# Kernel tuning notes

Hardware: AMD Instinct MI355X
Metric: run time of the kernel (lower is better)

## Reference

```python
import jax, jax.numpy as jnp
import numpy as np
from jax import lax

B, N, C = 16, 2304, 768
H_HEADS, D = 12, 64  # num_heads, head_dim
SCALE = 9.0 ** (-0.5)  # equivalent_head_dim ** -0.5


def setup_inputs() -> dict:
    key = jax.random.key(0)
    ks = jax.random.split(key, 8)
    return {
        "x": jax.random.normal(ks[0], (B, N, C), dtype=jnp.float32),
        "qkv_w": jax.random.normal(ks[1], (3 * C + 3 * D, C), dtype=jnp.float32) * 0.02,
        "qkv_b": jax.random.normal(ks[2], (3 * C + 3 * D,), dtype=jnp.float32) * 0.02,
        "w1": jax.random.normal(ks[3], (1, H_HEADS, D, D), dtype=jnp.float32) * 0.02,
        "w2": jax.random.normal(ks[4], (1, H_HEADS, D, D), dtype=jnp.float32) * 0.02,
        "w3": jax.random.normal(ks[5], (D, 1, 3, 3), dtype=jnp.float32) * 0.02,
        "proj_w": jax.random.normal(ks[6], (C, C + D), dtype=jnp.float32) * 0.02,
        "proj_b": jax.random.normal(ks[7], (C,), dtype=jnp.float32) * 0.02,
        "h": 48,
        "w": 48,
    }


def _inner_swiglu(k, v, w1, w2, lr=1.0):
    # k, v: [B, H, N, d]; w1, w2: [1, H, d, d]
    z1 = jnp.einsum('bhnd,hde->bhne', k, w1[0])
    z2 = jnp.einsum('bhnd,hde->bhne', k, w2[0])
    sig = jax.nn.sigmoid(z2)
    a = z2 * sig
    e = -v / float(v.shape[2]) * SCALE
    g1 = jnp.einsum('bhnd,bhne->bhde', k, e * a)
    g2 = jnp.einsum('bhnd,bhne->bhde', k, e * z1 * (sig * (1.0 + z2 * (1.0 - sig))))
    g1 = g1 / (jnp.linalg.norm(g1, axis=-2, keepdims=True) + 1.0)
    g2 = g2 / (jnp.linalg.norm(g2, axis=-2, keepdims=True) + 1.0)
    return w1 - lr * g1, w2 - lr * g2  # [B, H, d, d]


def _inner_3x3dwc(k, v, w3, hh, ww, lr=1.0):
    # k, v: [B, d, h, w]; w3: [d, 1, 3, 3]
    b, c = k.shape[0], k.shape[1]
    e = -v / float(hh * ww) * SCALE
    kp = jnp.pad(k, ((0, 0), (0, 0), (1, 1), (1, 1)))
    dots = []
    for ys in (0, 1, 2):  # 1 + dy
        for xs in (0, 1, 2):  # 1 + dx
            dots.append(jnp.sum(kp[:, :, ys:ys + hh, xs:xs + ww] * e, axis=(-2, -1)))
    g = jnp.stack(dots, axis=-1).reshape(b * c, 1, 3, 3)
    g = g / (jnp.sqrt(jnp.sum(g * g, axis=(-2, -1), keepdims=True)) + 1.0)
    return jnp.tile(w3, (b, 1, 1, 1)) - lr * g  # [B*d, 1, 3, 3]


def reference(x, qkv_w, qkv_b, w1, w2, w3, proj_w, proj_b, h, w):
    b, n, c = x.shape
    nh = w1.shape[1]
    d = c // nh
    qkv = x @ qkv_w.T + qkv_b  # [B, N, 3C + 3d]
    q1, k1, v1, q2, k2, v2 = jnp.split(
        qkv, [c, 2 * c, 3 * c, 3 * c + d, 3 * c + 2 * d], axis=-1)
    heads = lambda t: t.reshape(b, n, nh, d).transpose(0, 2, 1, 3)
    q1, k1, v1 = heads(q1), heads(k1), heads(v1)

    w1u, w2u = _inner_swiglu(k1, v1, w1, w2)
    x1 = jnp.einsum('bhnd,bhde->bhne', q1, w1u) * jax.nn.silu(
        jnp.einsum('bhnd,bhde->bhne', q1, w2u))
    x1 = x1.transpose(0, 2, 1, 3).reshape(b, n, c)

    spatial = lambda t: t.reshape(b, h, w, d).transpose(0, 3, 1, 2)  # [B, d, h, w]
    q2s, k2s, v2s = spatial(q2), spatial(k2), spatial(v2)
    w3u = _inner_3x3dwc(k2s, v2s, w3, h, w)
    x2 = lax.conv_general_dilated(
        q2s.reshape(1, b * d, h, w), w3u,
        window_strides=(1, 1), padding=((1, 1), (1, 1)),
        feature_group_count=b * d,
        dimension_numbers=('NCHW', 'OIHW', 'NCHW'))
    x2 = x2.reshape(b, d, n).transpose(0, 2, 1)  # [B, N, d]

    out = jnp.concatenate([x1, x2], axis=-1) @ proj_w.T + proj_b
    return out
```

## Files before the change

kernel.cpp:

```cpp
#include <hip/hip_runtime.h>
#include <hip/hip_bf16.h>
#include <math.h>

#define B_   16
#define N_   2304
#define C_   768
#define H_   12
#define D_   64
#define M_   (B_*N_)
#define NQKV 2496
#define NPAD 2560
#define CCP  896
#define EVS  (-1.0f/6912.0f)

typedef __bf16 bf16x8 __attribute__((ext_vector_type(8)));
typedef __bf16 bf16x4 __attribute__((ext_vector_type(4)));
typedef float  f32x4  __attribute__((ext_vector_type(4)));

static __device__ __forceinline__ void gload_lds16(const void* g, void* l) {
  __builtin_amdgcn_global_load_lds((const __attribute__((address_space(1))) void*)g,
                                   (__attribute__((address_space(3))) void*)l, 16, 0, 0);
}

static __device__ __forceinline__ bf16x8 ld8(const __bf16* p) {
  bf16x4 lo = *(const bf16x4*)p;
  bf16x4 hi = *(const bf16x4*)(p + 4);
  return __builtin_shufflevector(lo, hi, 0,1,2,3,4,5,6,7);
}

__global__ __launch_bounds__(256) void cvt_x(const float* __restrict__ in,
                                             __bf16* __restrict__ out, int n8) {
  int i = blockIdx.x * 256 + threadIdx.x;
  if (i >= n8) return;
  const float4* p = (const float4*)(in + (size_t)i * 8);
  float4 a = p[0], b = p[1];
  bf16x8 o = {(__bf16)a.x,(__bf16)a.y,(__bf16)a.z,(__bf16)a.w,
              (__bf16)b.x,(__bf16)b.y,(__bf16)b.z,(__bf16)b.w};
  *(bf16x8*)(out + (size_t)i * 8) = o;
}

__global__ __launch_bounds__(256) void cvt_wqkv(const float* __restrict__ w,
    const float* __restrict__ bias, __bf16* __restrict__ wout, float* __restrict__ bout) {
  int i = blockIdx.x * 256 + threadIdx.x;
  if (i < NPAD * 96) {
    int n = i / 96, c8 = i - n * 96;
    bf16x8 o;
    if (n < NQKV) {
      const float4* p = (const float4*)(w + (size_t)n * 768 + c8 * 8);
      float4 a = p[0], b = p[1];
      o = (bf16x8){(__bf16)a.x,(__bf16)a.y,(__bf16)a.z,(__bf16)a.w,
                   (__bf16)b.x,(__bf16)b.y,(__bf16)b.z,(__bf16)b.w};
    } else {
      o = (bf16x8){(__bf16)0.f,(__bf16)0.f,(__bf16)0.f,(__bf16)0.f,
                   (__bf16)0.f,(__bf16)0.f,(__bf16)0.f,(__bf16)0.f};
    }
    *(bf16x8*)(wout + (size_t)n * 768 + c8 * 8) = o;
  }
  if (i < NPAD) bout[i] = (i < NQKV) ? bias[i] : 0.0f;
}

__global__ __launch_bounds__(256) void cvt_pw(const float* __restrict__ in,
                                              __bf16* __restrict__ out) {
  int i = blockIdx.x * 256 + threadIdx.x;
  if (i >= 86016) return;
  int n = i / 112, c8 = i - n * 112;
  int k = c8 * 8;
  bf16x8 o;
  if (k < 832) {
    const float4* p = (const float4*)(in + (size_t)n * 832 + k);
    float4 a = p[0], b = p[1];
    o = (bf16x8){(__bf16)a.x,(__bf16)a.y,(__bf16)a.z,(__bf16)a.w,
                 (__bf16)b.x,(__bf16)b.y,(__bf16)b.z,(__bf16)b.w};
  } else {
    o = (bf16x8){(__bf16)0.f,(__bf16)0.f,(__bf16)0.f,(__bf16)0.f,
                 (__bf16)0.f,(__bf16)0.f,(__bf16)0.f,(__bf16)0.f};
  }
  *(bf16x8*)(out + (size_t)n * CCP + k) = o;
}

__global__ __launch_bounds__(256) void zeropad(__bf16* __restrict__ concat) {
  int i = blockIdx.x * 256 + threadIdx.x;
  if (i >= M_ * 8) return;
  int row = i >> 3, ch = i & 7;
  bf16x8 z = {(__bf16)0.f,(__bf16)0.f,(__bf16)0.f,(__bf16)0.f,
              (__bf16)0.f,(__bf16)0.f,(__bf16)0.f,(__bf16)0.f};
  *(bf16x8*)(concat + (size_t)row * CCP + 832 + ch * 8) = z;
}

template<int OUTF32>
__global__ __launch_bounds__(512, 2) void gemm8(
    const __bf16* __restrict__ A, const __bf16* __restrict__ Bt,
    const float* __restrict__ bias, void* __restrict__ Cout,
    const int K, const int ldc, const int nbn, const int KT)
{
  __shared__ __align__(16) __bf16 sA[2][2][128 * 64];
  __shared__ __align__(16) __bf16 sB[2][2][128 * 64];
  const int tid  = threadIdx.x;
  const int lane = tid & 63;
  const int wid  = tid >> 6;
  const int wm = wid >> 2;
  const int wn = wid & 3;
  const int l15 = lane & 15, lq = lane >> 4;

  const int nwg = gridDim.x;
  const int swz = ((int)blockIdx.x & 7) * (nwg >> 3) + ((int)blockIdx.x >> 3);
  const int bm = swz / nbn;
  const int bn = swz - bm * nbn;

  const int strow = tid >> 3;
  const int stoff = strow * 64 + (tid & 7) * 8;
  const __bf16* gA = A  + (size_t)((size_t)bm * 256 + strow) * K + ((tid & 7) ^ (strow & 7)) * 8;
  const __bf16* gB = Bt + (size_t)((size_t)bn * 256 + strow) * K + ((tid & 7) ^ (strow & 7)) * 8;

  f32x4 acc[2][4][2][2];
  #pragma unroll
  for (int a = 0; a < 2; ++a)
    #pragma unroll
    for (int m = 0; m < 4; ++m)
      #pragma unroll
      for (int b = 0; b < 2; ++b)
        #pragma unroll
        for (int n = 0; n < 2; ++n) acc[a][m][b][n] = (f32x4){0.f,0.f,0.f,0.f};

  bf16x8 af0[4][2], af1[4][2], bf0[2][2], bf1[2][2];

#define STAGE_A(q, h, T) do {                                                   \
    const size_t ko_ = (size_t)(T) * 64;                                        \
    gload_lds16(gA + (size_t)((h)*128 +  0) * K + ko_, &sA[q][h][stoff]);       \
    gload_lds16(gA + (size_t)((h)*128 + 64) * K + ko_, &sA[q][h][4096 + stoff]);\
  } while (0)
#define STAGE_B(q, h, T) do {                                                   \
    const size_t ko_ = (size_t)(T) * 64;                                        \
    gload_lds16(gB + (size_t)((h)*128 +  0) * K + ko_, &sB[q][h][stoff]);       \
    gload_lds16(gB + (size_t)((h)*128 + 64) * K + ko_, &sB[q][h][4096 + stoff]);\
  } while (0)
#define LOADA(DST, h, q) do {                                                   \
    _Pragma("unroll") for (int mf_ = 0; mf_ < 4; ++mf_) {                       \
      const int r_ = wm * 64 + mf_ * 16 + l15;                                  \
      _Pragma("unroll") for (int kk_ = 0; kk_ < 2; ++kk_)                       \
        DST[mf_][kk_] = *(const bf16x8*)&sA[q][h][r_ * 64 + (((kk_*4+lq) ^ (r_&7)) * 8)]; \
    } } while (0)
#define LOADB(DST, h, q) do {                                                   \
    _Pragma("unroll") for (int nf_ = 0; nf_ < 2; ++nf_) {                       \
      const int c_ = wn * 32 + nf_ * 16 + l15;                                  \
      _Pragma("unroll") for (int kk_ = 0; kk_ < 2; ++kk_)                       \
        DST[nf_][kk_] = *(const bf16x8*)&sB[q][h][c_ * 64 + (((kk_*4+lq) ^ (c_&7)) * 8)]; \
    } } while (0)
#define MMA(a_, b_, AF, BF) do {                                                \
    __builtin_amdgcn_s_setprio(1);                                              \
    _Pragma("unroll") for (int kk_ = 0; kk_ < 2; ++kk_)                         \
    _Pragma("unroll") for (int mf_ = 0; mf_ < 4; ++mf_)                         \
    _Pragma("unroll") for (int nf_ = 0; nf_ < 2; ++nf_)                         \
      acc[a_][mf_][b_][nf_] = __builtin_amdgcn_mfma_f32_16x16x32_bf16(          \
          AF[mf_][kk_], BF[nf_][kk_], acc[a_][mf_][b_][nf_], 0, 0, 0);          \
    __builtin_amdgcn_s_setprio(0);                                              \
  } while (0)
#define BAR  __builtin_amdgcn_s_barrier()
#define LGKM do { asm volatile("s_waitcnt lgkmcnt(0)" ::: "memory");            \
                  __builtin_amdgcn_sched_barrier(0); } while (0)
#define VMW4 asm volatile("s_waitcnt vmcnt(4)" ::: "memory")
#define VMW0 asm volatile("s_waitcnt vmcnt(0)" ::: "memory")

  STAGE_A(0, 0, 0); STAGE_A(0, 1, 0); STAGE_B(0, 0, 0); STAGE_B(0, 1, 0);
  STAGE_B(1, 0, 1);
  STAGE_A(1, 1, 1);
  VMW4;
  BAR;

  for (int t = 0; t < KT; t += 2) {
    LOADA(af0, 0, 0); LOADB(bf0, 0, 0);
    STAGE_A(1, 0, t + 1); STAGE_B(1, 1, t + 1);
    BAR; LGKM; MMA(0, 0, af0, bf0); BAR;
    LOADA(af1, 1, 0);
    BAR; LGKM; MMA(1, 0, af1, bf0); BAR;
    LOADB(bf1, 1, 0);
    if (t + 2 < KT) STAGE_B(0, 0, t + 2);
    BAR; LGKM; MMA(1, 1, af1, bf1); BAR;
    if (t + 2 < KT) STAGE_A(0, 1, t + 2);
    BAR; MMA(0, 1, af0, bf1);
    if (t + 2 < KT) { VMW4; } else { VMW0; }
    BAR;
    LOADA(af0, 0, 1); LOADB(bf0, 0, 1);
    if (t + 2 < KT) { STAGE_A(0, 0, t + 2); STAGE_B(0, 1, t + 2); }
    BAR; LGKM; MMA(0, 0, af0, bf0); BAR;
    LOADA(af1, 1, 1);
    BAR; LGKM; MMA(1, 0, af1, bf0); BAR;
    LOADB(bf1, 1, 1);
    if (t + 3 < KT) STAGE_B(1, 0, t + 3);
    BAR; LGKM; MMA(1, 1, af1, bf1); BAR;
    if (t + 3 < KT) STAGE_A(1, 1, t + 3);
    BAR; MMA(0, 1, af0, bf1);
    if (t + 3 < KT) { VMW4; } else { VMW0; }
    BAR;
  }
#undef STAGE_A
#undef STAGE_B
#undef LOADA
#undef LOADB
#undef MMA

  #pragma unroll
  for (int b = 0; b < 2; ++b)
    #pragma unroll
    for (int nf = 0; nf < 2; ++nf) {
      const int col = bn * 256 + b * 128 + wn * 32 + nf * 16 + l15;
      const float bs = bias[col];
      #pragma unroll
      for (int a = 0; a < 2; ++a)
        #pragma unroll
        for (int mf = 0; mf < 4; ++mf) {
          const int row0 = bm * 256 + a * 128 + wm * 64 + mf * 16 + lq * 4;
          #pragma unroll
          for (int r = 0; r < 4; ++r) {
            float v = acc[a][mf][b][nf][r] + bs;
            if (OUTF32) ((float*)Cout)[(size_t)(row0 + r) * ldc + col] = v;
            else        ((__bf16*)Cout)[(size_t)(row0 + r) * ldc + col] = (__bf16)v;
          }
        }
    }
}

__global__ __launch_bounds__(256, 2) void inner_swiglu(
    const __bf16* __restrict__ qkv, const float* __restrict__ w1,
    const float* __restrict__ w2, __bf16* __restrict__ concat)
{
  const int bh = blockIdx.x;
  const int b = bh / H_, h = bh - b * H_;
  const int tid = threadIdx.x, wid = tid >> 6, lane = tid & 63;
  const int wr = wid >> 1, wc = wid & 1, l15 = lane & 15, lq = lane >> 4;

  __shared__ __bf16 w1T[64 * 72], w2T[64 * 72];
  __shared__ union U {
    struct { __bf16 kN[64 * 72], kT[64 * 72], t1T[64 * 72], t2T[64 * 72]; } c;
    struct { float g1[64 * 65], g2[64 * 65]; float nrm1[64], nrm2[64]; } g;
  } u;

  const float* w1p = w1 + h * 4096;
  const float* w2p = w2 + h * 4096;
  for (int idx = tid; idx < 4096; idx += 256) {
    int d = idx >> 6, e = idx & 63;
    w1T[e * 72 + d] = (__bf16)w1p[idx];
    w2T[e * 72 + d] = (__bf16)w2p[idx];
  }

  f32x4 g1a[2][2], g2a[2][2];
  #pragma unroll
  for (int i = 0; i < 2; ++i)
    #pragma unroll
    for (int j = 0; j < 2; ++j) { g1a[i][j] = (f32x4){0.f,0.f,0.f,0.f}; g2a[i][j] = (f32x4){0.f,0.f,0.f,0.f}; }

  const size_t rowb = (size_t)b * N_;
  const int koff = C_ + h * D_;
  const int voff = 2 * C_ + h * D_;
  __syncthreads();

  const int sn = tid >> 2, sdb = tid & 3;

  for (int ci = 0; ci < 36; ++ci) {
    const int n0 = ci * 64;
    {
      const __bf16* src = qkv + (rowb + n0 + sn) * (size_t)NPAD + koff + sdb * 16;
      bf16x8 va = *(const bf16x8*)src;
      bf16x8 vb = *(const bf16x8*)(src + 8);
      __bf16* kn = &u.c.kN[sn * 72 + sdb * 16];
      *(bf16x4*)(kn + 0)  = __builtin_shufflevector(va, va, 0,1,2,3);
      *(bf16x4*)(kn + 4)  = __builtin_shufflevector(va, va, 4,5,6,7);
      *(bf16x4*)(kn + 8)  = __builtin_shufflevector(vb, vb, 0,1,2,3);
      *(bf16x4*)(kn + 12) = __builtin_shufflevector(vb, vb, 4,5,6,7);
      #pragma unroll
      for (int j = 0; j < 8; ++j) u.c.kT[(sdb * 16 + j) * 72 + sn] = va[j];
      #pragma unroll
      for (int j = 0; j < 8; ++j) u.c.kT[(sdb * 16 + 8 + j) * 72 + sn] = vb[j];
    }
    __syncthreads();

    f32x4 z1[2][2], z2[2][2];
    #pragma unroll
    for (int i = 0; i < 2; ++i)
      #pragma unroll
      for (int j = 0; j < 2; ++j) { z1[i][j] = (f32x4){0.f,0.f,0.f,0.f}; z2[i][j] = (f32x4){0.f,0.f,0.f,0.f}; }
    #pragma unroll
    for (int kk = 0; kk < 2; ++kk) {
      bf16x8 af[2], b1[2], b2[2];
      #pragma unroll
      for (int mi = 0; mi < 2; ++mi)
        af[mi] = ld8(&u.c.kN[(wr * 32 + mi * 16 + l15) * 72 + kk * 32 + lq * 8]);
      #pragma unroll
      for (int ni = 0; ni < 2; ++ni) {
        int e = wc * 32 + ni * 16 + l15;
        b1[ni] = ld8(&w1T[e * 72 + kk * 32 + lq * 8]);
        b2[ni] = ld8(&w2T[e * 72 + kk * 32 + lq * 8]);
      }
      #pragma unroll
      for (int mi = 0; mi < 2; ++mi)
        #pragma unroll
        for (int ni = 0; ni < 2; ++ni) {
          z1[mi][ni] = __builtin_amdgcn_mfma_f32_16x16x32_bf16(af[mi], b1[ni], z1[mi][ni], 0, 0, 0);
          z2[mi][ni] = __builtin_amdgcn_mfma_f32_16x16x32_bf16(af[mi], b2[ni], z2[mi][ni], 0, 0, 0);
        }
    }

    #pragma unroll
    for (int mi = 0; mi < 2; ++mi)
      #pragma unroll
      for (int ni = 0; ni < 2; ++ni) {
        int nl = wr * 32 + mi * 16 + lq * 4;
        int e  = wc * 32 + ni * 16 + l15;
        const __bf16* vp = qkv + (rowb + n0 + nl) * (size_t)NPAD + voff + e;
        #pragma unroll
        for (int r = 0; r < 4; ++r) {
          float vv  = (float)vp[(size_t)r * NPAD];
          float ev  = vv * EVS;
          float z1v = z1[mi][ni][r], z2v = z2[mi][ni][r];
          float sg  = 1.0f / (1.0f + __expf(-z2v));
          float t1  = ev * (z2v * sg);
          float t2  = ev * z1v * (sg * (1.0f + z2v * (1.0f - sg)));
          u.c.t1T[e * 72 + nl + r] = (__bf16)t1;
          u.c.t2T[e * 72 + nl + r] = (__bf16)t2;
        }
      }
    __syncthreads();

    #pragma unroll
    for (int kk = 0; kk < 2; ++kk) {
      bf16x8 af[2], b1[2], b2[2];
      #pragma unroll
      for (int mi = 0; mi < 2; ++mi)
        af[mi] = ld8(&u.c.kT[(wr * 32 + mi * 16 + l15) * 72 + kk * 32 + lq * 8]);
      #pragma unroll
      for (int ni = 0; ni < 2; ++ni) {
        int e = wc * 32 + ni * 16 + l15;
        b1[ni] = ld8(&u.c.t1T[e * 72 + kk * 32 + lq * 8]);
        b2[ni] = ld8(&u.c.t2T[e * 72 + kk * 32 + lq * 8]);
      }
      #pragma unroll
      for (int mi = 0; mi < 2; ++mi)
        #pragma unroll
        for (int ni = 0; ni < 2; ++ni) {
          g1a[mi][ni] = __builtin_amdgcn_mfma_f32_16x16x32_bf16(af[mi], b1[ni], g1a[mi][ni], 0, 0, 0);
          g2a[mi][ni] = __builtin_amdgcn_mfma_f32_16x16x32_bf16(af[mi], b2[ni], g2a[mi][ni], 0, 0, 0);
        }
    }
    __syncthreads();
  }

  #pragma unroll
  for (int mi = 0; mi < 2; ++mi)
    #pragma unroll
    for (int ni = 0; ni < 2; ++ni)
      #pragma unroll
      for (int r = 0; r < 4; ++r) {
        int d = wr * 32 + mi * 16 + lq * 4 + r;
        int e = wc * 32 + ni * 16 + l15;
        u.g.g1[d * 65 + e] = g1a[mi][ni][r];
        u.g.g2[d * 65 + e] = g2a[mi][ni][r];
      }
  __syncthreads();
  if (tid < 128) {
    const float* gs = (tid < 64) ? u.g.g1 : u.g.g2;
    int e = tid & 63;
    float s = 0.f;
    for (int d = 0; d < 64; ++d) { float gv = gs[d * 65 + e]; s += gv * gv; }
    float rn = 1.0f / (sqrtf(s) + 1.0f);
    if (tid < 64) u.g.nrm1[e] = rn; else u.g.nrm2[e] = rn;
  }
  __syncthreads();
  for (int idx = tid; idx < 4096; idx += 256) {
    int d = idx >> 6, e = idx & 63;
    float wu1 = w1p[idx] - u.g.g1[d * 65 + e] * u.g.nrm1[e];
    float wu2 = w2p[idx] - u.g.g2[d * 65 + e] * u.g.nrm2[e];
    w1T[e * 72 + d] = (__bf16)wu1;
    w2T[e * 72 + d] = (__bf16)wu2;
  }
  __syncthreads();

  const int qoff = h * D_;
  for (int ci = 0; ci < 36; ++ci) {
    const int n0 = ci * 64;
    {
      const __bf16* src = qkv + (rowb + n0 + sn) * (size_t)NPAD + qoff + sdb * 16;
      bf16x8 va = *(const bf16x8*)src;
      bf16x8 vb = *(const bf16x8*)(src + 8);
      __bf16* kn = &u.c.kN[sn * 72 + sdb * 16];
      *(bf16x4*)(kn + 0)  = __builtin_shufflevector(va, va, 0,1,2,3);
      *(bf16x4*)(kn + 4)  = __builtin_shufflevector(va, va, 4,5,6,7);
      *(bf16x4*)(kn + 8)  = __builtin_shufflevector(vb, vb, 0,1,2,3);
      *(bf16x4*)(kn + 12) = __builtin_shufflevector(vb, vb, 4,5,6,7);
    }
    __syncthreads();
    f32x4 y1[2][2], y2[2][2];
    #pragma unroll
    for (int i = 0; i < 2; ++i)
      #pragma unroll
      for (int j = 0; j < 2; ++j) { y1[i][j] = (f32x4){0.f,0.f,0.f,0.f}; y2[i][j] = (f32x4){0.f,0.f,0.f,0.f}; }
    #pragma unroll
    for (int kk = 0; kk < 2; ++kk) {
      bf16x8 af[2], b1[2], b2[2];
      #pragma unroll
      for (int mi = 0; mi < 2; ++mi)
        af[mi] = ld8(&u.c.kN[(wr * 32 + mi * 16 + l15) * 72 + kk * 32 + lq * 8]);
      #pragma unroll
      for (int ni = 0; ni < 2; ++ni) {
        int e = wc * 32 + ni * 16 + l15;
        b1[ni] = ld8(&w1T[e * 72 + kk * 32 + lq * 8]);
        b2[ni] = ld8(&w2T[e * 72 + kk * 32 + lq * 8]);
      }
      #pragma unroll
      for (int mi = 0; mi < 2; ++mi)
        #pragma unroll
        for (int ni = 0; ni < 2; ++ni) {
          y1[mi][ni] = __builtin_amdgcn_mfma_f32_16x16x32_bf16(af[mi], b1[ni], y1[mi][ni], 0, 0, 0);
          y2[mi][ni] = __builtin_amdgcn_mfma_f32_16x16x32_bf16(af[mi], b2[ni], y2[mi][ni], 0, 0, 0);
        }
    }
    #pragma unroll
    for (int mi = 0; mi < 2; ++mi)
      #pragma unroll
      for (int ni = 0; ni < 2; ++ni) {
        int nl = wr * 32 + mi * 16 + lq * 4;
        int e  = wc * 32 + ni * 16 + l15;
        #pragma unroll
        for (int r = 0; r < 4; ++r) {
          float a1 = y1[mi][ni][r], a2 = y2[mi][ni][r];
          float sg = 1.0f / (1.0f + __expf(-a2));
          concat[(rowb + n0 + nl + r) * (size_t)CCP + h * D_ + e] = (__bf16)(a1 * (a2 * sg));
        }
      }
    __syncthreads();
  }
}

__global__ __launch_bounds__(256) void dwc_grad(const __bf16* __restrict__ qkv,
    const float* __restrict__ w3, float* __restrict__ w3u) {
  int bd = blockIdx.x, b = bd >> 6, dd = bd & 63;
  int tid = threadIdx.x;
  __shared__ float kpad[50 * 50];
  __shared__ float red[9][4];
  for (int i = tid; i < 2500; i += 256) kpad[i] = 0.f;
  __syncthreads();
  const size_t base = (size_t)b * N_ * NPAD;
  for (int p = tid; p < 2304; p += 256) {
    int y = p / 48, x = p - y * 48;
    kpad[(y + 1) * 50 + x + 1] = (float)qkv[base + (size_t)p * NPAD + 2368 + dd];
  }
  __syncthreads();
  float acc[9];
  #pragma unroll
  for (int j = 0; j < 9; ++j) acc[j] = 0.f;
  for (int p = tid; p < 2304; p += 256) {
    int y = p / 48, x = p - y * 48;
    float e = (float)qkv[base + (size_t)p * NPAD + 2432 + dd] * EVS;
    #pragma unroll
    for (int j = 0; j < 9; ++j) {
      int ys = j / 3, xs = j - ys * 3;
      acc[j] += kpad[(y + ys) * 50 + (x + xs)] * e;
    }
  }
  #pragma unroll
  for (int j = 0; j < 9; ++j)
    for (int off = 32; off; off >>= 1) acc[j] += __shfl_down(acc[j], off);
  if ((tid & 63) == 0) {
    #pragma unroll
    for (int j = 0; j < 9; ++j) red[j][tid >> 6] = acc[j];
  }
  __syncthreads();
  if (tid == 0) {
    float g[9]; float ss = 0.f;
    #pragma unroll
    for (int j = 0; j < 9; ++j) {
      g[j] = red[j][0] + red[j][1] + red[j][2] + red[j][3];
      ss += g[j] * g[j];
    }
    float rn = 1.0f / (sqrtf(ss) + 1.0f);
    #pragma unroll
    for (int j = 0; j < 9; ++j) w3u[bd * 9 + j] = w3[dd * 9 + j] - g[j] * rn;
  }
}

__global__ __launch_bounds__(256) void dwc_apply(const __bf16* __restrict__ qkv,
    const float* __restrict__ w3u, __bf16* __restrict__ concat) {
  int bd = blockIdx.x, b = bd >> 6, dd = bd & 63;
  int tid = threadIdx.x;
  __shared__ float qpad[50 * 50];
  for (int i = tid; i < 2500; i += 256) qpad[i] = 0.f;
  __syncthreads();
  const size_t base = (size_t)b * N_ * NPAD;
  for (int p = tid; p < 2304; p += 256) {
    int y = p / 48, x = p - y * 48;
    qpad[(y + 1) * 50 + x + 1] = (float)qkv[base + (size_t)p * NPAD + 2304 + dd];
  }
  __syncthreads();
  float wv[9];
  #pragma unroll
  for (int j = 0; j < 9; ++j) wv[j] = w3u[bd * 9 + j];
  for (int p = tid; p < 2304; p += 256) {
    int y = p / 48, x = p - y * 48;
    float s = 0.f;
    #pragma unroll
    for (int j = 0; j < 9; ++j) {
      int ys = j / 3, xs = j - ys * 3;
      s += qpad[(y + ys) * 50 + (x + xs)] * wv[j];
    }
    concat[((size_t)b * N_ + p) * CCP + 768 + dd] = (__bf16)s;
  }
}

extern "C" void kernel_launch(void* const* d_in, const int* in_sizes, int n_in,
                              void* d_out, int out_size, void* d_ws, size_t ws_size,
                              hipStream_t stream) {
  const float* x      = (const float*)d_in[0];
  const float* qkv_w  = (const float*)d_in[1];
  const float* qkv_b  = (const float*)d_in[2];
  const float* w1     = (const float*)d_in[3];
  const float* w2     = (const float*)d_in[4];
  const float* w3     = (const float*)d_in[5];
  const float* proj_w = (const float*)d_in[6];
  const float* proj_b = (const float*)d_in[7];

  char* ws = (char*)d_ws;
  __bf16* xb     = (__bf16*)ws;
  __bf16* wqkvb  = (__bf16*)(ws + 56623104);
  float*  qkvbp  = (float*) (ws + 60555264);
  __bf16* concat = (__bf16*)ws;
  __bf16* qkvb16 = (__bf16*)(ws + 66060288);
  __bf16* pwb    = (__bf16*)(ws + 254803968);
  float*  w3u    = (float*) (ws + 256180224);

  cvt_x   <<<13824, 256, 0, stream>>>(x, xb, 3538944);
  cvt_wqkv<<<  960, 256, 0, stream>>>(qkv_w, qkv_b, wqkvb, qkvbp);
  cvt_pw  <<<  336, 256, 0, stream>>>(proj_w, pwb);

  gemm8<0><<<1440, 512, 0, stream>>>(xb, wqkvb, qkvbp, (void*)qkvb16,
                                     768, NPAD, 10, 12);

  zeropad<<<1152, 256, 0, stream>>>(concat);
  inner_swiglu<<<192, 256, 0, stream>>>(qkvb16, w1, w2, concat);
  dwc_grad <<<1024, 256, 0, stream>>>(qkvb16, w3, w3u);
  dwc_apply<<<1024, 256, 0, stream>>>(qkvb16, w3u, concat);

  gemm8<1><<<432, 512, 0, stream>>>(concat, pwb, proj_b, d_out,
                                    CCP, 768, 3, 14);
}
```

Baseline: 485.3 us.

## Rework GEMM wait scheduling, split swiglu over two groups, retile depthwise conv kernels

Three separate changes. The GEMM main loop drops its explicit lgkmcnt waits and puts sched_barrier fences after barriers and vmcnt waits. inner_swiglu moves to 512 threads, with two wave groups handling alternate 64-token chunks; V is staged through LDS, and the two groups' gradient partials are summed in shared memory. The depthwise conv gradient and apply kernels change from one block per (batch, channel) with strided scalar loads to blocks over 4-row spatial strips that read all 64 channels with vectorized loads, plus a small reduction kernel for the per-strip partial gradients. Removing the lgkmcnt waits leaves it to the compiler to wait for the LDS fragment loads before the MFMAs, which carries a correctness risk.

```diff
diff --git a/kernel.cpp b/kernel.cpp
--- a/kernel.cpp
+++ b/kernel.cpp
@@ -155,11 +155,12 @@
           AF[mf_][kk_], BF[nf_][kk_], acc[a_][mf_][b_][nf_], 0, 0, 0);          \
     __builtin_amdgcn_s_setprio(0);                                              \
   } while (0)
-#define BAR  __builtin_amdgcn_s_barrier()
-#define LGKM do { asm volatile("s_waitcnt lgkmcnt(0)" ::: "memory");            \
+#define BAR  do { __builtin_amdgcn_s_barrier();                                 \
                   __builtin_amdgcn_sched_barrier(0); } while (0)
-#define VMW4 asm volatile("s_waitcnt vmcnt(4)" ::: "memory")
-#define VMW0 asm volatile("s_waitcnt vmcnt(0)" ::: "memory")
+#define VMW4 do { asm volatile("s_waitcnt vmcnt(4)" ::: "memory");              \
+                  __builtin_amdgcn_sched_barrier(0); } while (0)
+#define VMW0 do { asm volatile("s_waitcnt vmcnt(0)" ::: "memory");              \
+                  __builtin_amdgcn_sched_barrier(0); } while (0)
 
   STAGE_A(0, 0, 0); STAGE_A(0, 1, 0); STAGE_B(0, 0, 0); STAGE_B(0, 1, 0);
   STAGE_B(1, 0, 1);
@@ -170,24 +171,24 @@
   for (int t = 0; t < KT; t += 2) {
     LOADA(af0, 0, 0); LOADB(bf0, 0, 0);
     STAGE_A(1, 0, t + 1); STAGE_B(1, 1, t + 1);
-    BAR; LGKM; MMA(0, 0, af0, bf0); BAR;
+    BAR; MMA(0, 0, af0, bf0); BAR;
     LOADA(af1, 1, 0);
-    BAR; LGKM; MMA(1, 0, af1, bf0); BAR;
+    BAR; MMA(1, 0, af1, bf0); BAR;
     LOADB(bf1, 1, 0);
     if (t + 2 < KT) STAGE_B(0, 0, t + 2);
-    BAR; LGKM; MMA(1, 1, af1, bf1); BAR;
+    BAR; MMA(1, 1, af1, bf1); BAR;
     if (t + 2 < KT) STAGE_A(0, 1, t + 2);
     BAR; MMA(0, 1, af0, bf1);
     if (t + 2 < KT) { VMW4; } else { VMW0; }
     BAR;
     LOADA(af0, 0, 1); LOADB(bf0, 0, 1);
     if (t + 2 < KT) { STAGE_A(0, 0, t + 2); STAGE_B(0, 1, t + 2); }
-    BAR; LGKM; MMA(0, 0, af0, bf0); BAR;
+    BAR; MMA(0, 0, af0, bf0); BAR;
     LOADA(af1, 1, 1);
-    BAR; LGKM; MMA(1, 0, af1, bf0); BAR;
+    BAR; MMA(1, 0, af1, bf0); BAR;
     LOADB(bf1, 1, 1);
     if (t + 3 < KT) STAGE_B(1, 0, t + 3);
-    BAR; LGKM; MMA(1, 1, af1, bf1); BAR;
+    BAR; MMA(1, 1, af1, bf1); BAR;
     if (t + 3 < KT) STAGE_A(1, 1, t + 3);
     BAR; MMA(0, 1, af0, bf1);
     if (t + 3 < KT) { VMW4; } else { VMW0; }
@@ -220,24 +221,27 @@
     }
 }
 
-__global__ __launch_bounds__(256, 2) void inner_swiglu(
+__global__ __launch_bounds__(512, 1) void inner_swiglu(
     const __bf16* __restrict__ qkv, const float* __restrict__ w1,
     const float* __restrict__ w2, __bf16* __restrict__ concat)
 {
   const int bh = blockIdx.x;
   const int b = bh / H_, h = bh - b * H_;
   const int tid = threadIdx.x, wid = tid >> 6, lane = tid & 63;
-  const int wr = wid >> 1, wc = wid & 1, l15 = lane & 15, lq = lane >> 4;
+  const int grp = wid >> 2;
+  const int wid2 = wid & 3;
+  const int wr = wid2 >> 1, wc = wid2 & 1, l15 = lane & 15, lq = lane >> 4;
 
   __shared__ __bf16 w1T[64 * 72], w2T[64 * 72];
   __shared__ union U {
-    struct { __bf16 kN[64 * 72], kT[64 * 72], t1T[64 * 72], t2T[64 * 72]; } c;
+    struct { __bf16 kN[2][64 * 72], kT[2][64 * 72], vN[2][64 * 72],
+                    t1T[2][64 * 72], t2T[2][64 * 72]; } c;
     struct { float g1[64 * 65], g2[64 * 65]; float nrm1[64], nrm2[64]; } g;
   } u;
 
   const float* w1p = w1 + h * 4096;
   const float* w2p = w2 + h * 4096;
-  for (int idx = tid; idx < 4096; idx += 256) {
+  for (int idx = tid; idx < 4096; idx += 512) {
     int d = idx >> 6, e = idx & 63;
     w1T[e * 72 + d] = (__bf16)w1p[idx];
     w2T[e * 72 + d] = (__bf16)w2p[idx];
@@ -252,25 +256,31 @@
   const size_t rowb = (size_t)b * N_;
   const int koff = C_ + h * D_;
   const int voff = 2 * C_ + h * D_;
-  __syncthreads();
-
-  const int sn = tid >> 2, sdb = tid & 3;
-
-  for (int ci = 0; ci < 36; ++ci) {
-    const int n0 = ci * 64;
+  const int st = tid & 255, sn = st >> 2, sdb = st & 3;
+
+  for (int it = 0; it < 18; ++it) {
+    const int n0 = (it * 2 + grp) * 64;
     {
       const __bf16* src = qkv + (rowb + n0 + sn) * (size_t)NPAD + koff + sdb * 16;
       bf16x8 va = *(const bf16x8*)src;
       bf16x8 vb = *(const bf16x8*)(src + 8);
-      __bf16* kn = &u.c.kN[sn * 72 + sdb * 16];
+      __bf16* kn = &u.c.kN[grp][sn * 72 + sdb * 16];
       *(bf16x4*)(kn + 0)  = __builtin_shufflevector(va, va, 0,1,2,3);
       *(bf16x4*)(kn + 4)  = __builtin_shufflevector(va, va, 4,5,6,7);
       *(bf16x4*)(kn + 8)  = __builtin_shufflevector(vb, vb, 0,1,2,3);
       *(bf16x4*)(kn + 12) = __builtin_shufflevector(vb, vb, 4,5,6,7);
       #pragma unroll
-      for (int j = 0; j < 8; ++j) u.c.kT[(sdb * 16 + j) * 72 + sn] = va[j];
-      #pragma unroll
-      for (int j = 0; j < 8; ++j) u.c.kT[(sdb * 16 + 8 + j) * 72 + sn] = vb[j];
+      for (int j = 0; j < 8; ++j) u.c.kT[grp][(sdb * 16 + j) * 72 + sn] = va[j];
+      #pragma unroll
+      for (int j = 0; j < 8; ++j) u.c.kT[grp][(sdb * 16 + 8 + j) * 72 + sn] = vb[j];
+      const __bf16* vsrc = qkv + (rowb + n0 + sn) * (size_t)NPAD + voff + sdb * 16;
+      bf16x8 wa = *(const bf16x8*)vsrc;
+      bf16x8 wb = *(const bf16x8*)(vsrc + 8);
+      __bf16* vn = &u.c.vN[grp][sn * 72 + sdb * 16];
+      *(bf16x4*)(vn + 0)  = __builtin_shufflevector(wa, wa, 0,1,2,3);
+      *(bf16x4*)(vn + 4)  = __builtin_shufflevector(wa, wa, 4,5,6,7);
+      *(bf16x4*)(vn + 8)  = __builtin_shufflevector(wb, wb, 0,1,2,3);
+      *(bf16x4*)(vn + 12) = __builtin_shufflevector(wb, wb, 4,5,6,7);
     }
     __syncthreads();
 
@@ -284,7 +294,7 @@
       bf16x8 af[2], b1[2], b2[2];
       #pragma unroll
       for (int mi = 0; mi < 2; ++mi)
-        af[mi] = ld8(&u.c.kN[(wr * 32 + mi * 16 + l15) * 72 + kk * 32 + lq * 8]);
+        af[mi] = ld8(&u.c.kN[grp][(wr * 32 + mi * 16 + l15) * 72 + kk * 32 + lq * 8]);
       #pragma unroll
       for (int ni = 0; ni < 2; ++ni) {
         int e = wc * 32 + ni * 16 + l15;
@@ -306,17 +316,16 @@
       for (int ni = 0; ni < 2; ++ni) {
         int nl = wr * 32 + mi * 16 + lq * 4;
         int e  = wc * 32 + ni * 16 + l15;
-        const __bf16* vp = qkv + (rowb + n0 + nl) * (size_t)NPAD + voff + e;
         #pragma unroll
         for (int r = 0; r < 4; ++r) {
-          float vv  = (float)vp[(size_t)r * NPAD];
+          float vv  = (float)u.c.vN[grp][(nl + r) * 72 + e];
           float ev  = vv * EVS;
           float z1v = z1[mi][ni][r], z2v = z2[mi][ni][r];
           float sg  = 1.0f / (1.0f + __expf(-z2v));
           float t1  = ev * (z2v * sg);
           float t2  = ev * z1v * (sg * (1.0f + z2v * (1.0f - sg)));
-          u.c.t1T[e * 72 + nl + r] = (__bf16)t1;
-          u.c.t2T[e * 72 + nl + r] = (__bf16)t2;
+          u.c.t1T[grp][e * 72 + nl + r] = (__bf16)t1;
+          u.c.t2T[grp][e * 72 + nl + r] = (__bf16)t2;
         }
       }
     __syncthreads();
@@ -326,12 +335,12 @@
       bf16x8 af[2], b1[2], b2[2];
       #pragma unroll
       for (int mi = 0; mi < 2; ++mi)
-        af[mi] = ld8(&u.c.kT[(wr * 32 + mi * 16 + l15) * 72 + kk * 32 + lq * 8]);
+        af[mi] = ld8(&u.c.kT[grp][(wr * 32 + mi * 16 + l15) * 72 + kk * 32 + lq * 8]);
       #pragma unroll
       for (int ni = 0; ni < 2; ++ni) {
         int e = wc * 32 + ni * 16 + l15;
-        b1[ni] = ld8(&u.c.t1T[e * 72 + kk * 32 + lq * 8]);
-        b2[ni] = ld8(&u.c.t2T[e * 72 + kk * 32 + lq * 8]);
+        b1[ni] = ld8(&u.c.t1T[grp][e * 72 + kk * 32 + lq * 8]);
+        b2[ni] = ld8(&u.c.t2T[grp][e * 72 + kk * 32 + lq * 8]);
       }
       #pragma unroll
       for (int mi = 0; mi < 2; ++mi)
@@ -344,17 +353,33 @@
     __syncthreads();
   }
 
-  #pragma unroll
-  for (int mi = 0; mi < 2; ++mi)
-    #pragma unroll
-    for (int ni = 0; ni < 2; ++ni)
-      #pragma unroll
-      for (int r = 0; r < 4; ++r) {
-        int d = wr * 32 + mi * 16 + lq * 4 + r;
-        int e = wc * 32 + ni * 16 + l15;
-        u.g.g1[d * 65 + e] = g1a[mi][ni][r];
-        u.g.g2[d * 65 + e] = g2a[mi][ni][r];
-      }
+  if (grp == 0) {
+    #pragma unroll
+    for (int mi = 0; mi < 2; ++mi)
+      #pragma unroll
+      for (int ni = 0; ni < 2; ++ni)
+        #pragma unroll
+        for (int r = 0; r < 4; ++r) {
+          int d = wr * 32 + mi * 16 + lq * 4 + r;
+          int e = wc * 32 + ni * 16 + l15;
+          u.g.g1[d * 65 + e] = g1a[mi][ni][r];
+          u.g.g2[d * 65 + e] = g2a[mi][ni][r];
+        }
+  }
+  __syncthreads();
+  if (grp == 1) {
+    #pragma unroll
+    for (int mi = 0; mi < 2; ++mi)
+      #pragma unroll
+      for (int ni = 0; ni < 2; ++ni)
+        #pragma unroll
+        for (int r = 0; r < 4; ++r) {
+          int d = wr * 32 + mi * 16 + lq * 4 + r;
+          int e = wc * 32 + ni * 16 + l15;
+          u.g.g1[d * 65 + e] += g1a[mi][ni][r];
+          u.g.g2[d * 65 + e] += g2a[mi][ni][r];
+        }
+  }
   __syncthreads();
   if (tid < 128) {
     const float* gs = (tid < 64) ? u.g.g1 : u.g.g2;
@@ -365,7 +390,7 @@
     if (tid < 64) u.g.nrm1[e] = rn; else u.g.nrm2[e] = rn;
   }
   __syncthreads();
-  for (int idx = tid; idx < 4096; idx += 256) {
+  for (int idx = tid; idx < 4096; idx += 512) {
     int d = idx >> 6, e = idx & 63;
     float wu1 = w1p[idx] - u.g.g1[d * 65 + e] * u.g.nrm1[e];
     float wu2 = w2p[idx] - u.g.g2[d * 65 + e] * u.g.nrm2[e];
@@ -375,13 +400,13 @@
   __syncthreads();
 
   const int qoff = h * D_;
-  for (int ci = 0; ci < 36; ++ci) {
-    const int n0 = ci * 64;
+  for (int it = 0; it < 18; ++it) {
+    const int n0 = (it * 2 + grp) * 64;
     {
       const __bf16* src = qkv + (rowb + n0 + sn) * (size_t)NPAD + qoff + sdb * 16;
       bf16x8 va = *(const bf16x8*)src;
       bf16x8 vb = *(const bf16x8*)(src + 8);
-      __bf16* kn = &u.c.kN[sn * 72 + sdb * 16];
+      __bf16* kn = &u.c.kN[grp][sn * 72 + sdb * 16];
       *(bf16x4*)(kn + 0)  = __builtin_shufflevector(va, va, 0,1,2,3);
       *(bf16x4*)(kn + 4)  = __builtin_shufflevector(va, va, 4,5,6,7);
       *(bf16x4*)(kn + 8)  = __builtin_shufflevector(vb, vb, 0,1,2,3);
@@ -398,7 +423,7 @@
       bf16x8 af[2], b1[2], b2[2];
       #pragma unroll
       for (int mi = 0; mi < 2; ++mi)
-        af[mi] = ld8(&u.c.kN[(wr * 32 + mi * 16 + l15) * 72 + kk * 32 + lq * 8]);
+        af[mi] = ld8(&u.c.kN[grp][(wr * 32 + mi * 16 + l15) * 72 + kk * 32 + lq * 8]);
       #pragma unroll
       for (int ni = 0; ni < 2; ++ni) {
         int e = wc * 32 + ni * 16 + l15;
@@ -430,77 +455,102 @@
   }
 }
 
-__global__ __launch_bounds__(256) void dwc_grad(const __bf16* __restrict__ qkv,
-    const float* __restrict__ w3, float* __restrict__ w3u) {
-  int bd = blockIdx.x, b = bd >> 6, dd = bd & 63;
-  int tid = threadIdx.x;
-  __shared__ float kpad[50 * 50];
-  __shared__ float red[9][4];
-  for (int i = tid; i < 2500; i += 256) kpad[i] = 0.f;
+__global__ __launch_bounds__(256) void dwc_grad2(const __bf16* __restrict__ qkv,
+                                                 float* __restrict__ w3p) {
+  const int blk = blockIdx.x;
+  const int b = blk / 12, sp = blk - b * 12;
+  const int tid = threadIdx.x, dd = tid & 63, rl = tid >> 6;
+  __shared__ __bf16 kS[6 * 50 * 64];
+  __shared__ float red[4][9][64];
+  for (int i = tid; i < 9600; i += 256) ((unsigned*)kS)[i] = 0u;
   __syncthreads();
   const size_t base = (size_t)b * N_ * NPAD;
-  for (int p = tid; p < 2304; p += 256) {
-    int y = p / 48, x = p - y * 48;
-    kpad[(y + 1) * 50 + x + 1] = (float)qkv[base + (size_t)p * NPAD + 2368 + dd];
+  for (int i = tid; i < 6 * 48 * 8; i += 256) {
+    int y6 = i / 384; int rem = i - y6 * 384; int x = rem >> 3; int c8 = rem & 7;
+    int y = 4 * sp - 1 + y6;
+    if (y >= 0 && y < 48) {
+      int p = y * 48 + x;
+      bf16x8 v = *(const bf16x8*)&qkv[base + (size_t)p * NPAD + 2368 + c8 * 8];
+      *(bf16x8*)&kS[((y6 * 50) + x + 1) * 64 + c8 * 8] = v;
+    }
   }
   __syncthreads();
   float acc[9];
   #pragma unroll
   for (int j = 0; j < 9; ++j) acc[j] = 0.f;
-  for (int p = tid; p < 2304; p += 256) {
-    int y = p / 48, x = p - y * 48;
+  const int y = 4 * sp + rl;
+  for (int x = 0; x < 48; ++x) {
+    int p = y * 48 + x;
     float e = (float)qkv[base + (size_t)p * NPAD + 2432 + dd] * EVS;
     #pragma unroll
     for (int j = 0; j < 9; ++j) {
       int ys = j / 3, xs = j - ys * 3;
-      acc[j] += kpad[(y + ys) * 50 + (x + xs)] * e;
-    }
-  }
-  #pragma unroll
-  for (int j = 0; j < 9; ++j)
-    for (int off = 32; off; off >>= 1) acc[j] += __shfl_down(acc[j], off);
-  if ((tid & 63) == 0) {
-    #pragma unroll
-    for (int j = 0; j < 9; ++j) red[j][tid >> 6] = acc[j];
-  }
-  __syncthreads();
-  if (tid == 0) {
-    float g[9]; float ss = 0.f;
+      acc[j] += (float)kS[((rl + ys) * 50 + x + xs) * 64 + dd] * e;
+    }
+  }
+  #pragma unroll
+  for (int j = 0; j < 9; ++j) red[rl][j][dd] = acc[j];
+  __syncthreads();
+  if (rl == 0) {
     #pragma unroll
     for (int j = 0; j < 9; ++j) {
-      g[j] = red[j][0] + red[j][1] + red[j][2] + red[j][3];
-      ss += g[j] * g[j];
-    }
-    float rn = 1.0f / (sqrtf(ss) + 1.0f);
-    #pragma unroll
-    for (int j = 0; j < 9; ++j) w3u[bd * 9 + j] = w3[dd * 9 + j] - g[j] * rn;
-  }
-}
-
-__global__ __launch_bounds__(256) void dwc_apply(const __bf16* __restrict__ qkv,
+      float s = red[0][j][dd] + red[1][j][dd] + red[2][j][dd] + red[3][j][dd];
+      w3p[((size_t)(b * 12 + sp) * 64 + dd) * 9 + j] = s;
+    }
+  }
+}
+
+__global__ __launch_bounds__(256) void dwc_upd(const float* __restrict__ w3p,
+    const float* __restrict__ w3, float* __restrict__ w3u) {
+  int i = blockIdx.x * 256 + threadIdx.x;
+  if (i >= 1024) return;
+  int b = i >> 6, dd = i & 63;
+  float g[9];
+  #pragma unroll
+  for (int j = 0; j < 9; ++j) g[j] = 0.f;
+  for (int sp = 0; sp < 12; ++sp)
+    #pragma unroll
+    for (int j = 0; j < 9; ++j)
+      g[j] += w3p[((size_t)(b * 12 + sp) * 64 + dd) * 9 + j];
+  float ss = 0.f;
+  #pragma unroll
+  for (int j = 0; j < 9; ++j) ss += g[j] * g[j];
+  float rn = 1.0f / (sqrtf(ss) + 1.0f);
+  #pragma unroll
+  for (int j = 0; j < 9; ++j) w3u[i * 9 + j] = w3[dd * 9 + j] - g[j] * rn;
+}
+
+__global__ __launch_bounds__(256) void dwc_apply2(const __bf16* __restrict__ qkv,
     const float* __restrict__ w3u, __bf16* __restrict__ concat) {
-  int bd = blockIdx.x, b = bd >> 6, dd = bd & 63;
-  int tid = threadIdx.x;
-  __shared__ float qpad[50 * 50];
-  for (int i = tid; i < 2500; i += 256) qpad[i] = 0.f;
+  const int blk = blockIdx.x;
+  const int b = blk / 12, sp = blk - b * 12;
+  const int tid = threadIdx.x, dd = tid & 63, rl = tid >> 6;
+  __shared__ __bf16 qS[6 * 50 * 64];
+  for (int i = tid; i < 9600; i += 256) ((unsigned*)qS)[i] = 0u;
   __syncthreads();
   const size_t base = (size_t)b * N_ * NPAD;
-  for (int p = tid; p < 2304; p += 256) {
-    int y = p / 48, x = p - y * 48;
-    qpad[(y + 1) * 50 + x + 1] = (float)qkv[base + (size_t)p * NPAD + 2304 + dd];
+  for (int i = tid; i < 6 * 48 * 8; i += 256) {
+    int y6 = i / 384; int rem = i - y6 * 384; int x = rem >> 3; int c8 = rem & 7;
+    int y = 4 * sp - 1 + y6;
+    if (y >= 0 && y < 48) {
+      int p = y * 48 + x;
+      bf16x8 v = *(const bf16x8*)&qkv[base + (size_t)p * NPAD + 2304 + c8 * 8];
+      *(bf16x8*)&qS[((y6 * 50) + x + 1) * 64 + c8 * 8] = v;
+    }
   }
   __syncthreads();
   float wv[9];
   #pragma unroll
-  for (int j = 0; j < 9; ++j) wv[j] = w3u[bd * 9 + j];
-  for (int p = tid; p < 2304; p += 256) {
-    int y = p / 48, x = p - y * 48;
+  for (int j = 0; j < 9; ++j) wv[j] = w3u[(size_t)(b * 64 + dd) * 9 + j];
+  const int y = 4 * sp + rl;
+  for (int x = 0; x < 48; ++x) {
     float s = 0.f;
     #pragma unroll
     for (int j = 0; j < 9; ++j) {
       int ys = j / 3, xs = j - ys * 3;
-      s += qpad[(y + ys) * 50 + (x + xs)] * wv[j];
-    }
+      s += (float)qS[((rl + ys) * 50 + x + xs) * 64 + dd] * wv[j];
+    }
+    int p = y * 48 + x;
     concat[((size_t)b * N_ + p) * CCP + 768 + dd] = (__bf16)s;
   }
 }
@@ -525,6 +575,7 @@
   __bf16* qkvb16 = (__bf16*)(ws + 66060288);
   __bf16* pwb    = (__bf16*)(ws + 254803968);
   float*  w3u    = (float*) (ws + 256180224);
+  float*  w3p    = (float*) (ws + 256217088);
 
   cvt_x   <<<13824, 256, 0, stream>>>(x, xb, 3538944);
   cvt_wqkv<<<  960, 256, 0, stream>>>(qkv_w, qkv_b, wqkvb, qkvbp);
@@ -534,9 +585,10 @@
                                      768, NPAD, 10, 12);
 
   zeropad<<<1152, 256, 0, stream>>>(concat);
-  inner_swiglu<<<192, 256, 0, stream>>>(qkvb16, w1, w2, concat);
-  dwc_grad <<<1024, 256, 0, stream>>>(qkvb16, w3, w3u);
-  dwc_apply<<<1024, 256, 0, stream>>>(qkvb16, w3u, concat);
+  inner_swiglu<<<192, 512, 0, stream>>>(qkvb16, w1, w2, concat);
+  dwc_grad2 <<<192, 256, 0, stream>>>(qkvb16, w3p);
+  dwc_upd   <<<  4, 256, 0, stream>>>(w3p, w3, w3u);
+  dwc_apply2<<<192, 256, 0, stream>>>(qkvb16, w3u, concat);
 
   gemm8<1><<<432, 512, 0, stream>>>(concat, pwb, proj_b, d_out,
                                     CCP, 768, 3, 14);
```

Result: faster. 453.2 us (-6.6%).
